# Kernel optimization log

Hardware: AMD Instinct MI355X
Metric: run time of the kernel (lower is better)

Reference implementation:

```python
import jax, jax.numpy as jnp
import numpy as np

B_, L_, DM = 2, 2048, 768        # batch, seq_len, d_model
DS, DC, EXP = 32, 7, 2           # d_state, d_conv, expand
DI = EXP * DM                    # d_inner = 1536
EPS = 1e-5


def setup_inputs() -> dict:
    key = jax.random.key(0)
    ks = jax.random.split(key, 6)
    sc = lambda k, shp: jax.random.normal(k, shp, jnp.float32) * 0.02
    x = jax.random.normal(ks[0], (B_, L_, DM), jnp.float32)
    Win = sc(ks[1], (2 * DI, DM))            # in_proj weight (no bias)
    conv_w = sc(ks[2], (DI, 1, DC))          # depthwise conv weight (O, I/groups, K)
    conv_b = jnp.zeros((DI,), jnp.float32)   # conv bias
    Wx = sc(ks[3], (2 * DS + DI, DI))        # x_proj weight (no bias)
    A_log = jnp.broadcast_to(jnp.log(jnp.arange(1, DS + 1, dtype=jnp.float32)), (DI, DS))
    D = jnp.ones((DI,), jnp.float32)
    Wout = sc(ks[4], (DM, DI))               # out_proj weight (no bias)
    ln_g = jnp.ones((DM,), jnp.float32)
    ln_b = jnp.zeros((DM,), jnp.float32)
    return {"x": x, "Win": Win, "conv_w": conv_w, "conv_b": conv_b, "Wx": Wx,
            "A_log": A_log, "D": D, "Wout": Wout, "ln_g": ln_g, "ln_b": ln_b}


def _mamba_forward(x, Win, conv_w, conv_b, Wx, A_log, D, Wout, ln_g, ln_b):
    residual = x
    # LayerNorm (biased variance, eps=1e-5)
    mu = jnp.mean(x, axis=-1, keepdims=True)
    var = jnp.var(x, axis=-1, keepdims=True)
    xn = (x - mu) / jnp.sqrt(var + EPS) * ln_g + ln_b
    # in_proj then split into x, z streams
    xz = xn @ Win.T                          # (b, l, 2*di)
    xc, z = jnp.split(xz, 2, axis=-1)
    # depthwise causal conv: pad (d_conv-1) left, truncate to L (matches torch pad+slice)
    xt = jnp.moveaxis(xc, 1, 2)              # (b, di, l)
    conv = jax.lax.conv_general_dilated(
        xt, conv_w, window_strides=(1,), padding=[(DC - 1, 0)],
        dimension_numbers=('NCH', 'OIH', 'NCH'), feature_group_count=DI)
    conv = conv + conv_b[None, :, None]
    xc = jax.nn.silu(jnp.moveaxis(conv, 1, 2))   # (b, l, di); dropout is identity (eval)
    # selective SSM
    xp = xc @ Wx.T                           # (b, l, 2*ds + di)
    Bm = xp[..., :DS]                        # (b, l, ds)
    Cm = xp[..., DS:2 * DS]                  # (b, l, ds)
    delta = jax.nn.softplus(xp[..., 2 * DS:])  # (b, l, di)
    A = -jnp.exp(A_log)                      # (di, ds)
    dA = jnp.exp(delta[..., None] * A)                       # (b, l, di, ds)
    dBx = (delta * xc)[..., None] * Bm[:, :, None, :]        # (b, l, di, ds)
    def step(h, inp):
        dA_t, dBx_t, C_t = inp
        h = dA_t * h + dBx_t                 # (b, di, ds)
        y = jnp.einsum('bdn,bn->bd', h, C_t)
        return h, y
    h0 = jnp.zeros((x.shape[0], DI, DS), xc.dtype)
    xs = (jnp.moveaxis(dA, 1, 0), jnp.moveaxis(dBx, 1, 0), jnp.moveaxis(Cm, 1, 0))
    _, ys = jax.lax.scan(step, h0, xs)       # (l, b, di)
    y = jnp.moveaxis(ys, 0, 1) + xc * D      # (b, l, di)
    # gated output, out_proj, residual
    y = y * jax.nn.silu(z)
    return y @ Wout.T + residual


def reference(x, Win, conv_w, conv_b, Wx, A_log, D, Wout, ln_g, ln_b):
    return _mamba_forward(x, Win, conv_w, conv_b, Wx, A_log, D, Wout, ln_g, ln_b)
```

## Files before the change

kernel.cpp:

```cpp
#include <hip/hip_runtime.h>
#include <hip/hip_bf16.h>

#define B_  2
#define L_  2048
#define DM  768
#define DS  32
#define DC  7
#define DI  1536
#define NTOK (B_*L_)
#define N1  (2*DI)
#define N2  (2*DS+DI)
#define N2P 1664
#define NC  64
#define CL  (L_/NC)
#define DGRP (DI/256)

using bf16 = __hip_bfloat16;
typedef short  short8 __attribute__((ext_vector_type(8)));
typedef short  s16x4  __attribute__((ext_vector_type(4)));
typedef float  f32x4  __attribute__((ext_vector_type(4)));
typedef unsigned u32x4 __attribute__((ext_vector_type(4)));

__device__ __forceinline__ float b2f(bf16 h) { return __bfloat162float(h); }
__device__ __forceinline__ bf16  f2b(float f){ return __float2bfloat16(f); }
__device__ __forceinline__ short bfbits(float f){ bf16 h = f2b(f); return *(short*)&h; }
__device__ __forceinline__ float bits2f(short s){ bf16 h; *(short*)&h = s; return b2f(h); }

__device__ __forceinline__ float exp2fast(float x) {
#if __has_builtin(__builtin_amdgcn_exp2f)
    return __builtin_amdgcn_exp2f(x);
#else
    return __expf(x * 0.6931471805599453f);
#endif
}

__global__ void detect_flag(const unsigned* __restrict__ lng, unsigned* __restrict__ flag)
{
    if (threadIdx.x == 0 && blockIdx.x == 0)
        *flag = (lng[0] == 0x3F800000u) ? 1u : 0u;
}

struct CvtArgs {
    const void* src[10];
    bf16*       dst[10];
    int         n[10];
    int         total;
};

__global__ __launch_bounds__(256) void convert_all(CvtArgs a, const unsigned* __restrict__ flag)
{
    int i = blockIdx.x * 256 + threadIdx.x;
    if (i >= a.total) return;
    int k = 0;
#pragma unroll
    for (int s = 0; s < 10; ++s) {
        if (i >= a.n[s]) { i -= a.n[s]; k = s + 1; }
        else break;
    }
    if (k >= 10) return;
    if (*flag) a.dst[k][i] = f2b(((const float*)a.src[k])[i]);
    else       a.dst[k][i] = ((const bf16*)a.src[k])[i];
}

__global__ __launch_bounds__(256) void ln_kernel(const bf16* __restrict__ x,
                                                 const bf16* __restrict__ g,
                                                 const bf16* __restrict__ b,
                                                 bf16* __restrict__ xn)
{
    int row = blockIdx.x;
    int t   = threadIdx.x;
    const bf16* xr = x + (size_t)row * DM;

    float v[3];
    float s = 0.f, s2 = 0.f;
#pragma unroll
    for (int i = 0; i < 3; ++i) {
        float f = b2f(xr[t + i * 256]);
        v[i] = f; s += f; s2 += f * f;
    }
#pragma unroll
    for (int off = 32; off > 0; off >>= 1) {
        s  += __shfl_down(s,  off);
        s2 += __shfl_down(s2, off);
    }
    __shared__ float red[8];
    if ((t & 63) == 0) { red[(t >> 6) * 2] = s; red[(t >> 6) * 2 + 1] = s2; }
    __syncthreads();
    float S  = red[0] + red[2] + red[4] + red[6];
    float S2 = red[1] + red[3] + red[5] + red[7];
    float mu  = S * (1.f / DM);
    float var = S2 * (1.f / DM) - mu * mu;
    float inv = 1.f / sqrtf(var + 1e-5f);
#pragma unroll
    for (int i = 0; i < 3; ++i) {
        int col = t + i * 256;
        float o = (v[i] - mu) * inv * b2f(g[col]) + b2f(b[col]);
        xn[(size_t)row * DM + col] = f2b(o);
    }
}

template<int MODE, int BN, bool SWZ>
__global__ __launch_bounds__(256) void gemm_bt(const bf16* __restrict__ A,
                                               const bf16* __restrict__ W,
                                               void* __restrict__ Cout,
                                               const bf16* __restrict__ Res,
                                               int M, int N, int K, int LD,
                                               const unsigned* __restrict__ flag,
                                               float* __restrict__ BCf,
                                               bf16* __restrict__ dT)
{
    constexpr int BM = 128, BK = 32, PITCH = 40;
    constexpr int AU = BM * 4;
    constexpr int TU = (BM + BN) * 4;
    constexpr int NU = TU / 256;
    constexpr int MT = (BN == 128) ? 4 : 2;
    constexpr int NT = 4;
    __shared__ __align__(16) bf16 As[2][BM * PITCH];
    __shared__ __align__(16) bf16 Ws[2][BN * PITCH];

    int bx, by;
    if constexpr (SWZ) {
        int gx   = gridDim.x;
        int nwg  = gx * gridDim.y;
        int flat = blockIdx.y * gx + blockIdx.x;
        int swz  = (flat & 7) * (nwg >> 3) + (flat >> 3);
        bx = swz % gx; by = swz / gx;
    } else {
        bx = blockIdx.x; by = blockIdx.y;
    }

    int kh = 0;
    if (MODE == 4) {
        int mblocks = M / BM;
        kh  = by / mblocks;
        by  = by % mblocks;
    }
    int koff = kh * K;

    int t    = threadIdx.x;
    int m0   = by * BM;
    int n0   = bx * BN;
    int wave = t >> 6, lane = t & 63;
    int quad = lane >> 4, l16 = lane & 15;
    int wm   = (BN == 128) ? (wave >> 1) * 64 : wave * 32;
    int wn   = (BN == 128) ? (wave & 1) * 64 : 0;

    auto loadu = [&](int u, int k0) -> short8 {
        if (u < AU) {
            int row = u >> 2, cu = (u & 3) * 8;
            return *(const short8*)(A + (size_t)(m0 + row) * LD + koff + k0 + cu);
        } else {
            int v = u - AU;
            int row = v >> 2, cu = (v & 3) * 8;
            int nrow = n0 + row;
            short8 z = {0,0,0,0,0,0,0,0};
            if (nrow < N) z = *(const short8*)(W + (size_t)nrow * LD + koff + k0 + cu);
            return z;
        }
    };
    auto storeu = [&](int buf, int u, short8 v) {
        if (u < AU) {
            int row = u >> 2, cu = (u & 3) * 8;
            *(short8*)(&As[buf][row * PITCH + cu]) = v;
        } else {
            int w = u - AU;
            int row = w >> 2, cu = (w & 3) * 8;
            *(short8*)(&Ws[buf][row * PITCH + cu]) = v;
        }
    };

    f32x4 acc[MT][NT] = {};
    short8 prA[NU], prB[NU];

#pragma unroll
    for (int p = 0; p < NU; ++p) prA[p] = loadu(t + 256 * p, 0);
#pragma unroll
    for (int p = 0; p < NU; ++p) storeu(0, t + 256 * p, prA[p]);
#pragma unroll
    for (int p = 0; p < NU; ++p) prB[p] = loadu(t + 256 * p, BK);
    __syncthreads();

    auto compute = [&](int buf) {
        short8 af[MT], bfr[NT];
#pragma unroll
        for (int i = 0; i < MT; ++i)
            af[i]  = *(const short8*)(&As[buf][(wm + i * 16 + l16) * PITCH + quad * 8]);
#pragma unroll
        for (int i = 0; i < NT; ++i)
            bfr[i] = *(const short8*)(&Ws[buf][(wn + i * 16 + l16) * PITCH + quad * 8]);
#pragma unroll
        for (int mt = 0; mt < MT; ++mt)
#pragma unroll
            for (int nt = 0; nt < NT; ++nt)
                acc[mt][nt] = __builtin_amdgcn_mfma_f32_16x16x32_bf16(
                    af[mt], bfr[nt], acc[mt][nt], 0, 0, 0);
    };

    for (int k0 = 0; k0 < K; k0 += 2 * BK) {
        if (k0 + 2 * BK < K) {
#pragma unroll
            for (int p = 0; p < NU; ++p) prA[p] = loadu(t + 256 * p, k0 + 2 * BK);
        }
        compute(0);
        {
#pragma unroll
            for (int p = 0; p < NU; ++p) storeu(1, t + 256 * p, prB[p]);
            __syncthreads();
        }
        if (k0 + 3 * BK < K) {
#pragma unroll
            for (int p = 0; p < NU; ++p) prB[p] = loadu(t + 256 * p, k0 + 3 * BK);
        }
        compute(1);
        if (k0 + 2 * BK < K) {
#pragma unroll
            for (int p = 0; p < NU; ++p) storeu(0, t + 256 * p, prA[p]);
            __syncthreads();
        }
    }

    bool f32out = (MODE == 2) ? (*flag != 0u) : false;

    if (MODE == 3) {
        float* Bf = BCf;
        float* Cf = BCf + (size_t)NTOK * DS;
#pragma unroll
        for (int mt = 0; mt < MT; ++mt)
#pragma unroll
            for (int nt = 0; nt < NT; ++nt) {
                int row0 = m0 + wm + mt * 16 + quad * 4;
                int col  = n0 + wn + nt * 16 + l16;
                if (col >= N) continue;
                f32x4 v = acc[mt][nt];
                if (col < DS) {
#pragma unroll
                    for (int r = 0; r < 4; ++r)
                        Bf[(size_t)(row0 + r) * DS + col] = v[r];
                } else if (col < 2 * DS) {
#pragma unroll
                    for (int r = 0; r < 4; ++r)
                        Cf[(size_t)(row0 + r) * DS + (col - DS)] = v[r];
                } else {
                    int dcol = col - 2 * DS;
#pragma unroll
                    for (int r = 0; r < 4; ++r) {
                        float x = v[r];
                        float s = fmaxf(x, 0.f) + __logf(1.f + __expf(-fabsf(x)));
                        dT[(size_t)(row0 + r) * DI + dcol] = f2b(s);
                    }
                }
            }
        return;
    }

    if (MODE == 4) {
        float* P = (float*)Cout + (size_t)kh * M * N;
#pragma unroll
        for (int mt = 0; mt < MT; ++mt)
#pragma unroll
            for (int nt = 0; nt < NT; ++nt)
#pragma unroll
                for (int r = 0; r < 4; ++r) {
                    int row = m0 + wm + mt * 16 + quad * 4 + r;
                    int col = n0 + wn + nt * 16 + l16;
                    P[(size_t)row * N + col] = acc[mt][nt][r];
                }
        return;
    }

#pragma unroll
    for (int mt = 0; mt < MT; ++mt)
#pragma unroll
        for (int nt = 0; nt < NT; ++nt)
#pragma unroll
            for (int r = 0; r < 4; ++r) {
                int row = m0 + wm + mt * 16 + quad * 4 + r;
                int col = n0 + wn + nt * 16 + l16;
                if (col >= N) continue;
                float v = acc[mt][nt][r];
                size_t idx = (size_t)row * N + col;
                if (MODE == 0) {
                    ((bf16*)Cout)[idx] = f2b(v);
                } else {
                    v += b2f(Res[idx]);
                    if (f32out) ((float*)Cout)[idx] = v;
                    else        ((bf16*)Cout)[idx]  = f2b(v);
                }
            }
}

__global__ __launch_bounds__(256) void reduce2(const float* __restrict__ p0,
                                               const float* __restrict__ p1,
                                               const bf16* __restrict__ res,
                                               void* __restrict__ out,
                                               const unsigned* __restrict__ flag,
                                               int n4)
{
    int i = blockIdx.x * 256 + threadIdx.x;
    if (i >= n4) return;
    f32x4 a = ((const f32x4*)p0)[i];
    f32x4 b = ((const f32x4*)p1)[i];
    s16x4 rz = ((const s16x4*)res)[i];
    f32x4 v;
#pragma unroll
    for (int j = 0; j < 4; ++j) v[j] = a[j] + b[j] + bits2f(rz[j]);
    if (*flag) {
        ((f32x4*)out)[i] = v;
    } else {
        s16x4 o;
#pragma unroll
        for (int j = 0; j < 4; ++j) o[j] = bfbits(v[j]);
        ((s16x4*)out)[i] = o;
    }
}

#define CCB 32
#define CTW 64
__global__ __launch_bounds__(256) void conv_silu(const bf16* __restrict__ xz,
                                                 const bf16* __restrict__ w,
                                                 const bf16* __restrict__ bias,
                                                 bf16* __restrict__ xconv)
{
    const int nCB = DI / CCB;
    int blk = blockIdx.x;
    int d0  = (blk % nCB) * CCB;
    int g0b = (blk / nCB) * CTW;
    int t   = threadIdx.x;
    int cb  = t & 31;
    int tg  = t >> 5;
    int d   = d0 + cb;
    int g0  = g0b + tg * 8;
    int l0  = g0 % L_;

    float wv[DC];
#pragma unroll
    for (int k = 0; k < DC; ++k) wv[k] = b2f(w[d * DC + k]);
    float bs = b2f(bias[d]);

    float xh[14];
#pragma unroll
    for (int j = 0; j < 14; ++j) {
        int lloc = l0 - 6 + j;
        xh[j] = (lloc >= 0) ? b2f(xz[(size_t)(g0 - 6 + j) * N1 + d]) : 0.f;
    }

#pragma unroll
    for (int r = 0; r < 8; ++r) {
        float acc = bs;
#pragma unroll
        for (int k = 0; k < DC; ++k)
            acc += xh[r + k] * wv[k];
        float s = acc / (1.f + __expf(-acc));
        xconv[(size_t)(g0 + r) * DI + d] = f2b(s);
    }
}

__global__ __launch_bounds__(256) void scan_a(const float* __restrict__ Bf,
                                              const bf16* __restrict__ dT,
                                              const bf16* __restrict__ xc,
                                              const bf16* __restrict__ A_log,
                                              float* __restrict__ hend,
                                              float* __restrict__ sdbuf)
{
    int blk  = blockIdx.x;
    int dgrp = blk % DGRP;
    int bc   = blk / DGRP;
    int c    = bc % NC;
    int b    = bc / NC;
    int d    = dgrp * 256 + threadIdx.x;

    __shared__ float Bs[CL * DS];
    size_t tok0 = (size_t)b * L_ + (size_t)c * CL;
    ((f32x4*)Bs)[threadIdx.x] = ((const f32x4*)(Bf + tok0 * DS))[threadIdx.x];

    float a2[DS];
    {
        short8 al[4];
#pragma unroll
        for (int k = 0; k < 4; ++k) al[k] = *(const short8*)(A_log + d * DS + k * 8);
#pragma unroll
        for (int n = 0; n < DS; ++n)
            a2[n] = -__expf(bits2f(al[n >> 3][n & 7])) * 1.44269504f;
    }
    float h[DS];
#pragma unroll
    for (int n = 0; n < DS; ++n) h[n] = 0.f;
    float sd = 0.f;
    __syncthreads();

    float de_c = b2f(dT[tok0 * DI + d]);
    float xv_c = b2f(xc[tok0 * DI + d]);
    for (int t = 0; t < CL; ++t) {
        float de_n = de_c, xv_n = xv_c;
        if (t + 1 < CL) {
            de_n = b2f(dT[(tok0 + t + 1) * DI + d]);
            xv_n = b2f(xc[(tok0 + t + 1) * DI + d]);
        }
        float w = de_c * xv_c;
        sd += de_c;
#pragma unroll
        for (int n = 0; n < DS; ++n) {
            float Bn = Bs[t * DS + n];
            float dA = exp2fast(de_c * a2[n]);
            h[n] = fmaf(dA, h[n], w * Bn);
        }
        de_c = de_n; xv_c = xv_n;
    }
    size_t base = (size_t)bc * DS * DI + d;
#pragma unroll
    for (int n = 0; n < DS; ++n) hend[base + (size_t)n * DI] = h[n];
    sdbuf[(size_t)bc * DI + d] = sd;
}

__global__ __launch_bounds__(256) void scan_b(float* __restrict__ hend,
                                              const float* __restrict__ sdbuf,
                                              const bf16* __restrict__ A_log)
{
    int i = blockIdx.x * 256 + threadIdx.x;
    int d = i % DI;
    int r = i / DI;
    int n = r % DS;
    int b = r / DS;
    float a2 = -__expf(b2f(A_log[d * DS + n])) * 1.44269504f;
    float h = 0.f;
#pragma unroll 4
    for (int c = 0; c < NC; ++c) {
        int bc = b * NC + c;
        size_t idx = ((size_t)bc * DS + n) * DI + d;
        float he = hend[idx];
        float pa = exp2fast(a2 * sdbuf[(size_t)bc * DI + d]);
        hend[idx] = h;
        h = fmaf(pa, h, he);
    }
}

__global__ __launch_bounds__(256) void scan_c(const float* __restrict__ Bf,
                                              const float* __restrict__ Cf,
                                              const bf16* __restrict__ dT,
                                              const bf16* __restrict__ xc,
                                              const bf16* __restrict__ xz,
                                              const bf16* __restrict__ A_log,
                                              const bf16* __restrict__ Dp,
                                              const float* __restrict__ hin,
                                              bf16* __restrict__ yg)
{
    int blk  = blockIdx.x;
    int dgrp = blk % DGRP;
    int bc   = blk / DGRP;
    int c    = bc % NC;
    int b    = bc / NC;
    int d    = dgrp * 256 + threadIdx.x;

    __shared__ float Bs[CL * DS];
    __shared__ float Cs[CL * DS];
    size_t tok0 = (size_t)b * L_ + (size_t)c * CL;
    ((f32x4*)Bs)[threadIdx.x] = ((const f32x4*)(Bf + tok0 * DS))[threadIdx.x];
    ((f32x4*)Cs)[threadIdx.x] = ((const f32x4*)(Cf + tok0 * DS))[threadIdx.x];

    float a2[DS];
    {
        short8 al[4];
#pragma unroll
        for (int k = 0; k < 4; ++k) al[k] = *(const short8*)(A_log + d * DS + k * 8);
#pragma unroll
        for (int n = 0; n < DS; ++n)
            a2[n] = -__expf(bits2f(al[n >> 3][n & 7])) * 1.44269504f;
    }
    float h[DS];
    size_t hb = (size_t)bc * DS * DI + d;
#pragma unroll
    for (int n = 0; n < DS; ++n) h[n] = hin[hb + (size_t)n * DI];
    float Dd = b2f(Dp[d]);
    __syncthreads();

    float de_c = b2f(dT[tok0 * DI + d]);
    float xv_c = b2f(xc[tok0 * DI + d]);
    float zf_c = b2f(xz[tok0 * N1 + DI + d]);
    for (int t = 0; t < CL; ++t) {
        float de_n = de_c, xv_n = xv_c, zf_n = zf_c;
        if (t + 1 < CL) {
            size_t tn = tok0 + t + 1;
            de_n = b2f(dT[tn * DI + d]);
            xv_n = b2f(xc[tn * DI + d]);
            zf_n = b2f(xz[tn * N1 + DI + d]);
        }
        float w = de_c * xv_c;

        float ya[4] = {0.f, 0.f, 0.f, 0.f};
#pragma unroll
        for (int n = 0; n < DS; ++n) {
            float Bn  = Bs[t * DS + n];
            float Cnv = Cs[t * DS + n];
            float dA  = exp2fast(de_c * a2[n]);
            h[n] = fmaf(dA, h[n], w * Bn);
            ya[n & 3] = fmaf(h[n], Cnv, ya[n & 3]);
        }
        float y  = (ya[0] + ya[1]) + (ya[2] + ya[3]);
        float sz = zf_c / (1.f + __expf(-zf_c));
        yg[(tok0 + t) * DI + d] = f2b((y + xv_c * Dd) * sz);
        de_c = de_n; xv_c = xv_n; zf_c = zf_n;
    }
}

extern "C" void kernel_launch(void* const* d_in, const int* in_sizes, int n_in,
                              void* d_out, int out_size, void* d_ws, size_t ws_size,
                              hipStream_t stream)
{
    (void)in_sizes; (void)n_in; (void)out_size; (void)ws_size;

    char* ws = (char*)d_ws;
    size_t off = 0;
    auto alloc = [&](size_t bytes) -> char* {
        char* p = ws + off;
        off += (bytes + 255) & ~(size_t)255;
        return p;
    };

    unsigned* flag = (unsigned*)alloc(4);
    bf16*  xb     = (bf16*)alloc((size_t)NTOK * DM * 2);
    bf16*  Winb   = (bf16*)alloc((size_t)N1 * DM * 2);
    bf16*  convwb = (bf16*)alloc((size_t)DI * DC * 2);
    bf16*  convbb = (bf16*)alloc((size_t)DI * 2);
    bf16*  Wxb    = (bf16*)alloc((size_t)N2 * DI * 2);
    bf16*  Alogb  = (bf16*)alloc((size_t)DI * DS * 2);
    bf16*  Db     = (bf16*)alloc((size_t)DI * 2);
    bf16*  Woutb  = (bf16*)alloc((size_t)DM * DI * 2);
    bf16*  lngb   = (bf16*)alloc((size_t)DM * 2);
    bf16*  lnbb   = (bf16*)alloc((size_t)DM * 2);
    bf16*  xn     = (bf16*)alloc((size_t)NTOK * DM * 2);
    bf16*  xz     = (bf16*)alloc((size_t)NTOK * N1 * 2);
    bf16*  xconv  = (bf16*)alloc((size_t)NTOK * DI * 2);
    float* hend   = (float*)alloc((size_t)B_ * NC * DS * DI * 4);
    float* BCf    = (float*)alloc((size_t)2 * NTOK * DS * 4);
    bf16*  dTrm   = (bf16*)alloc((size_t)NTOK * DI * 2);
    bf16*  yg     = (bf16*)alloc((size_t)NTOK * DI * 2);
    float* sdbuf  = (float*)alloc((size_t)B_ * NC * DI * 4);
    float* g3p    = (float*)alloc((size_t)2 * NTOK * DM * 4);

    detect_flag<<<1, 64, 0, stream>>>((const unsigned*)d_in[8], flag);

    CvtArgs ca;
    const int ns[10] = { NTOK * DM, N1 * DM, DI * DC, DI, N2 * DI,
                         DI * DS, DI, DM * DI, DM, DM };
    bf16* ds[10] = { xb, Winb, convwb, convbb, Wxb, Alogb, Db, Woutb, lngb, lnbb };
    int total = 0;
    for (int k = 0; k < 10; ++k) {
        ca.src[k] = d_in[k];
        ca.dst[k] = ds[k];
        ca.n[k]   = ns[k];
        total    += ns[k];
    }
    ca.total = total;
    convert_all<<<(total + 255) / 256, 256, 0, stream>>>(ca, flag);

    ln_kernel<<<NTOK, 256, 0, stream>>>(xb, lngb, lnbb, xn);

    gemm_bt<0, 128, true><<<dim3(N1 / 128, NTOK / 128), 256, 0, stream>>>(
        xn, Winb, (void*)xz, nullptr, NTOK, N1, DM, DM, nullptr, nullptr, nullptr);

    conv_silu<<<(DI / CCB) * (NTOK / CTW), 256, 0, stream>>>(
        xz, convwb, convbb, xconv);

    gemm_bt<3, 128, false><<<dim3(N2P / 128, NTOK / 128), 256, 0, stream>>>(
        xconv, Wxb, nullptr, nullptr, NTOK, N2, DI, DI, nullptr, BCf, dTrm);

    scan_a<<<B_ * NC * DGRP, 256, 0, stream>>>(
        BCf, dTrm, xconv, Alogb, hend, sdbuf);
    scan_b<<<(B_ * DS * DI) / 256, 256, 0, stream>>>(hend, sdbuf, Alogb);
    scan_c<<<B_ * NC * DGRP, 256, 0, stream>>>(
        BCf, BCf + (size_t)NTOK * DS, dTrm, xconv, xz, Alogb, Db, hend, yg);

    gemm_bt<4, 64, true><<<dim3(DM / 64, 2 * (NTOK / 128)), 256, 0, stream>>>(
        yg, Woutb, (void*)g3p, nullptr, NTOK, DM, DI / 2, DI, nullptr, nullptr, nullptr);
    reduce2<<<(NTOK * DM / 4 + 255) / 256, 256, 0, stream>>>(
        g3p, g3p + (size_t)NTOK * DM, xb, d_out, flag, NTOK * DM / 4);
}
```

Before: 338.4 us.

## Store B/C interleaved as bf16 and read directly in scan kernels

```diff
diff --git a/kernel.cpp b/kernel.cpp
--- a/kernel.cpp
+++ b/kernel.cpp
@@ -106,7 +106,7 @@
                                                const bf16* __restrict__ Res,
                                                int M, int N, int K, int LD,
                                                const unsigned* __restrict__ flag,
-                                               float* __restrict__ BCf,
+                                               bf16* __restrict__ BCb,
                                                bf16* __restrict__ dT)
 {
     constexpr int BM = 128, BK = 32, PITCH = 40;
@@ -222,8 +222,6 @@
     bool f32out = (MODE == 2) ? (*flag != 0u) : false;
 
     if (MODE == 3) {
-        float* Bf = BCf;
-        float* Cf = BCf + (size_t)NTOK * DS;
 #pragma unroll
         for (int mt = 0; mt < MT; ++mt)
 #pragma unroll
@@ -235,11 +233,11 @@
                 if (col < DS) {
 #pragma unroll
                     for (int r = 0; r < 4; ++r)
-                        Bf[(size_t)(row0 + r) * DS + col] = v[r];
+                        BCb[(size_t)(row0 + r) * (2 * DS) + 2 * col] = f2b(v[r]);
                 } else if (col < 2 * DS) {
 #pragma unroll
                     for (int r = 0; r < 4; ++r)
-                        Cf[(size_t)(row0 + r) * DS + (col - DS)] = v[r];
+                        BCb[(size_t)(row0 + r) * (2 * DS) + 2 * (col - DS) + 1] = f2b(v[r]);
                 } else {
                     int dcol = col - 2 * DS;
 #pragma unroll
@@ -355,7 +353,7 @@
     }
 }
 
-__global__ __launch_bounds__(256) void scan_a(const float* __restrict__ Bf,
+__global__ __launch_bounds__(256) void scan_a(const unsigned* __restrict__ BC32,
                                               const bf16* __restrict__ dT,
                                               const bf16* __restrict__ xc,
                                               const bf16* __restrict__ A_log,
@@ -369,10 +367,6 @@
     int b    = bc / NC;
     int d    = dgrp * 256 + threadIdx.x;
 
-    __shared__ float Bs[CL * DS];
-    size_t tok0 = (size_t)b * L_ + (size_t)c * CL;
-    ((f32x4*)Bs)[threadIdx.x] = ((const f32x4*)(Bf + tok0 * DS))[threadIdx.x];
-
     float a2[DS];
     {
         short8 al[4];
@@ -386,11 +380,16 @@
 #pragma unroll
     for (int n = 0; n < DS; ++n) h[n] = 0.f;
     float sd = 0.f;
-    __syncthreads();
+
+    size_t tok0 = (size_t)b * L_ + (size_t)c * CL;
+    const u32x4* qp = (const u32x4*)(BC32 + tok0 * DS);
 
     float de_c = b2f(dT[tok0 * DI + d]);
     float xv_c = b2f(xc[tok0 * DI + d]);
     for (int t = 0; t < CL; ++t) {
+        u32x4 q[8];
+#pragma unroll
+        for (int k = 0; k < 8; ++k) q[k] = qp[t * 8 + k];
         float de_n = de_c, xv_n = xv_c;
         if (t + 1 < CL) {
             de_n = b2f(dT[(tok0 + t + 1) * DI + d]);
@@ -400,7 +399,7 @@
         sd += de_c;
 #pragma unroll
         for (int n = 0; n < DS; ++n) {
-            float Bn = Bs[t * DS + n];
+            float Bn = __uint_as_float(q[n >> 2][n & 3] << 16);
             float dA = exp2fast(de_c * a2[n]);
             h[n] = fmaf(dA, h[n], w * Bn);
         }
@@ -434,8 +433,7 @@
     }
 }
 
-__global__ __launch_bounds__(256) void scan_c(const float* __restrict__ Bf,
-                                              const float* __restrict__ Cf,
+__global__ __launch_bounds__(256) void scan_c(const unsigned* __restrict__ BC32,
                                               const bf16* __restrict__ dT,
                                               const bf16* __restrict__ xc,
                                               const bf16* __restrict__ xz,
@@ -451,12 +449,6 @@
     int b    = bc / NC;
     int d    = dgrp * 256 + threadIdx.x;
 
-    __shared__ float Bs[CL * DS];
-    __shared__ float Cs[CL * DS];
-    size_t tok0 = (size_t)b * L_ + (size_t)c * CL;
-    ((f32x4*)Bs)[threadIdx.x] = ((const f32x4*)(Bf + tok0 * DS))[threadIdx.x];
-    ((f32x4*)Cs)[threadIdx.x] = ((const f32x4*)(Cf + tok0 * DS))[threadIdx.x];
-
     float a2[DS];
     {
         short8 al[4];
@@ -471,12 +463,17 @@
 #pragma unroll
     for (int n = 0; n < DS; ++n) h[n] = hin[hb + (size_t)n * DI];
     float Dd = b2f(Dp[d]);
-    __syncthreads();
+
+    size_t tok0 = (size_t)b * L_ + (size_t)c * CL;
+    const u32x4* qp = (const u32x4*)(BC32 + tok0 * DS);
 
     float de_c = b2f(dT[tok0 * DI + d]);
     float xv_c = b2f(xc[tok0 * DI + d]);
     float zf_c = b2f(xz[tok0 * N1 + DI + d]);
     for (int t = 0; t < CL; ++t) {
+        u32x4 q[8];
+#pragma unroll
+        for (int k = 0; k < 8; ++k) q[k] = qp[t * 8 + k];
         float de_n = de_c, xv_n = xv_c, zf_n = zf_c;
         if (t + 1 < CL) {
             size_t tn = tok0 + t + 1;
@@ -489,8 +486,9 @@
         float ya[4] = {0.f, 0.f, 0.f, 0.f};
 #pragma unroll
         for (int n = 0; n < DS; ++n) {
-            float Bn  = Bs[t * DS + n];
-            float Cnv = Cs[t * DS + n];
+            unsigned dw = q[n >> 2][n & 3];
+            float Bn  = __uint_as_float(dw << 16);
+            float Cnv = __uint_as_float(dw & 0xFFFF0000u);
             float dA  = exp2fast(de_c * a2[n]);
             h[n] = fmaf(dA, h[n], w * Bn);
             ya[n & 3] = fmaf(h[n], Cnv, ya[n & 3]);
@@ -531,7 +529,7 @@
     bf16*  xz     = (bf16*)alloc((size_t)NTOK * N1 * 2);
     bf16*  xconv  = (bf16*)alloc((size_t)NTOK * DI * 2);
     float* hend   = (float*)alloc((size_t)B_ * NC * DS * DI * 4);
-    float* BCf    = (float*)alloc((size_t)2 * NTOK * DS * 4);
+    bf16*  BCb    = (bf16*)alloc((size_t)NTOK * 2 * DS * 2);
     bf16*  dTrm   = (bf16*)alloc((size_t)NTOK * DI * 2);
     bf16*  yg     = (bf16*)alloc((size_t)NTOK * DI * 2);
     float* sdbuf  = (float*)alloc((size_t)B_ * NC * DI * 4);
@@ -562,13 +560,13 @@
         xz, convwb, convbb, xconv);
 
     gemm_bt<3, 128, false><<<dim3(N2P / 128, NTOK / 128), 256, 0, stream>>>(
-        xconv, Wxb, nullptr, nullptr, NTOK, N2, DI, DI, nullptr, BCf, dTrm);
+        xconv, Wxb, nullptr, nullptr, NTOK, N2, DI, DI, nullptr, BCb, dTrm);
 
     scan_a<<<B_ * NC * DGRP, 256, 0, stream>>>(
-        BCf, dTrm, xconv, Alogb, hend, sdbuf);
+        (const unsigned*)BCb, dTrm, xconv, Alogb, hend, sdbuf);
     scan_b<<<(B_ * DS * DI) / 256, 256, 0, stream>>>(hend, sdbuf, Alogb);
     scan_c<<<B_ * NC * DGRP, 256, 0, stream>>>(
-        BCf, BCf + (size_t)NTOK * DS, dTrm, xconv, xz, Alogb, Db, hend, yg);
+        (const unsigned*)BCb, dTrm, xconv, xz, Alogb, Db, hend, yg);
 
     gemm_bt<4, 64, true><<<dim3(DM / 64, 2 * (NTOK / 128)), 256, 0, stream>>>(
         yg, Woutb, (void*)g3p, nullptr, NTOK, DM, DI / 2, DI, nullptr, nullptr, nullptr);
```

Result: slower. 346.8 us (+2.5%).
